# Performance work log

Hardware: AMD Instinct MI355X
Metric: run time of the kernel (lower is better)

The kernel has to match this reference:

```python
import jax, jax.numpy as jnp
import numpy as np

N = 100000
E = 1600000
IN_DIM = 128
HID_DIM = 128
OUT_DIM = 128


def _sage_conv(x, src, dst, W_l, b_l, W_r, num_nodes):
    """PyG SAGEConv with mean aggregation:
       out = mean_{j in N(i)} x_j @ W_l + b_l + x_i @ W_r
    edge_index convention: messages flow src -> dst."""
    msg = x[src]                                        # [E, d_in] gather
    agg_sum = jax.ops.segment_sum(msg, dst, num_segments=num_nodes)   # [N, d_in]
    cnt = jax.ops.segment_sum(jnp.ones((msg.shape[0],), x.dtype), dst,
                              num_segments=num_nodes)   # [N]
    agg = agg_sum / jnp.maximum(cnt, 1.0)[:, None]      # scatter-mean (0 for isolated nodes)
    return agg @ W_l + b_l + x @ W_r


def setup_inputs() -> dict:
    key = jax.random.key(0)
    ks = jax.random.split(key, 8)
    def glorot(k, fan_in, fan_out):
        s = jnp.sqrt(2.0 / (fan_in + fan_out))
        return jax.random.normal(k, (fan_in, fan_out), dtype=jnp.float32) * s
    x = jax.random.normal(ks[0], (N, IN_DIM), dtype=jnp.float32)
    edge_index = jax.random.randint(ks[1], (2, E), 0, N, dtype=jnp.int64)
    return {
        "x": x,
        "edge_index": edge_index,
        "W1_l": glorot(ks[2], IN_DIM, HID_DIM),
        "b1": jnp.zeros((HID_DIM,), jnp.float32),
        "W1_r": glorot(ks[3], IN_DIM, HID_DIM),
        "W2_l": glorot(ks[4], HID_DIM, OUT_DIM),
        "b2": jnp.zeros((OUT_DIM,), jnp.float32),
        "W2_r": glorot(ks[5], HID_DIM, OUT_DIM),
    }


def reference(x, edge_index, W1_l, b1, W1_r, W2_l, b2, W2_r):
    src, dst = edge_index[0], edge_index[1]
    h = _sage_conv(x, src, dst, W1_l, b1, W1_r, N)
    h = jax.nn.relu(h)
    # F.dropout(p=0.5, training=self.training): identity in eval mode
    out = _sage_conv(h, src, dst, W2_l, b2, W2_r, N)
    return out
```

## Files before the change

kernel.cpp:

```cpp
#include <hip/hip_runtime.h>
#include <hip/hip_bf16.h>

#define N_NODES 100000
#define N_EDGES 1600000
#define DIM 128
#define BR 32
#define ESTG 1024
#define NB 782
#define CHUNK 16384

typedef __attribute__((ext_vector_type(8))) short bf16x8;
typedef __attribute__((ext_vector_type(4))) float f32x4;
typedef __attribute__((ext_vector_type(2))) float f32x2;

#define OFF_ROWPTR 0
#define OFF_BCNT   (N_NODES + 4)
#define OFF_BBASE  (OFF_BCNT + NB)
#define OFF_BCUR   (OFF_BBASE + NB)
#define OFF_PAIRS  (OFF_BCUR + NB)
#define OFF_COLSRC (OFF_PAIRS + N_EDGES)
#define OFF_HB     (OFF_COLSRC + N_EDGES)
#define OFF_HF8    (OFF_HB + N_NODES * DIM / 2)
#define OFF_WB     (OFF_HF8 + N_NODES * DIM / 4)

__device__ inline unsigned int f2bf(float f) {
    unsigned int u = __float_as_uint(f);
    return (u + 0x7FFFu + ((u >> 16) & 1u)) >> 16;
}

__global__ __launch_bounds__(256) void conv_pack_kernel(
    const float* __restrict__ x, unsigned char* __restrict__ xf8,
    const float* __restrict__ W1l, const float* __restrict__ W1r,
    const float* __restrict__ W2l, const float* __restrict__ W2r,
    unsigned short* __restrict__ WB,
    const int* __restrict__ dst, int* __restrict__ bcnt)
{
    __shared__ int histL[NB];
    const int b = blockIdx.x;
    const int tid = threadIdx.x;
    if (b < 6250) {
        long i = (long)(b * 256 + tid) * 8;
        float4 a = *(const float4*)(x + i);
        float4 c = *(const float4*)(x + i + 4);
        unsigned int w0 = 0, w1 = 0;
        w0 = __builtin_amdgcn_cvt_pk_fp8_f32(a.x, a.y, w0, false);
        w0 = __builtin_amdgcn_cvt_pk_fp8_f32(a.z, a.w, w0, true);
        w1 = __builtin_amdgcn_cvt_pk_fp8_f32(c.x, c.y, w1, false);
        w1 = __builtin_amdgcn_cvt_pk_fp8_f32(c.z, c.w, w1, true);
        uint2 o; o.x = w0; o.y = w1;
        *(uint2*)(xf8 + i) = o;
    } else if (b < 6506) {
        int t = (b - 6250) * 256 + tid;
        int layer = t >> 15;
        int rest  = t & 32767;
        int half  = rest >> 14;
        int idx   = rest & 16383;
        int k = idx >> 7;
        int n = idx & 127;
        const float* W = layer ? (half ? W2r : W2l) : (half ? W1r : W1l);
        int kk = half * 128 + k;
        WB[layer * 32768 + (((kk >> 3) * 128 + n) << 3) + (kk & 7)] =
            (unsigned short)f2bf(W[idx]);
    } else {
        const int e0 = (b - 6506) * CHUNK;
        const int e1 = min(e0 + CHUNK, N_EDGES);
        for (int q = tid; q < NB; q += 256) histL[q] = 0;
        __syncthreads();
        for (int i = e0 + tid; i < e1; i += 256)
            atomicAdd(&histL[dst[i] >> 7], 1);
        __syncthreads();
        for (int q = tid; q < NB; q += 256) {
            int c = histL[q];
            if (c) atomicAdd(&bcnt[q], c);
        }
    }
}

__global__ __launch_bounds__(1024) void bscan_kernel(
    const int* __restrict__ bcnt, int* __restrict__ bbase,
    int* __restrict__ bcur, int* __restrict__ rowptr)
{
    __shared__ int tmp[1024];
    int tid = threadIdx.x;
    int v = (tid < NB) ? bcnt[tid] : 0;
    tmp[tid] = v;
    __syncthreads();
    for (int off = 1; off < 1024; off <<= 1) {
        int t = (tid >= off) ? tmp[tid - off] : 0;
        __syncthreads();
        tmp[tid] += t;
        __syncthreads();
    }
    if (tid < NB) { int b = tmp[tid] - v; bbase[tid] = b; bcur[tid] = b; }
    if (tid == 0) rowptr[N_NODES] = N_EDGES;
}

__global__ __launch_bounds__(256) void bfill_kernel(
    const int* __restrict__ src, const int* __restrict__ dst,
    int* __restrict__ bcur, unsigned int* __restrict__ pairs)
{
    __shared__ int histL[NB];
    __shared__ int baseL[NB];
    const int tid = threadIdx.x;
    const int e0 = blockIdx.x * CHUNK;
    const int e1 = min(e0 + CHUNK, N_EDGES);
    for (int b = tid; b < NB; b += 256) histL[b] = 0;
    __syncthreads();
    for (int i = e0 + tid; i < e1; i += 256)
        atomicAdd(&histL[dst[i] >> 7], 1);
    __syncthreads();
    for (int b = tid; b < NB; b += 256) {
        int c = histL[b];
        baseL[b] = c ? atomicAdd(&bcur[b], c) : 0;
        histL[b] = 0;
    }
    __syncthreads();
    for (int i = e0 + tid; i < e1; i += 256) {
        int s = src[i];
        int d = dst[i];
        int bk = d >> 7;
        int r = atomicAdd(&histL[bk], 1);
        pairs[baseL[bk] + r] = (unsigned int)s | ((unsigned int)(d & 127) << 25);
    }
}

__global__ __launch_bounds__(256) void bucket_csr_kernel(
    const unsigned int* __restrict__ pairs,
    const int* __restrict__ bcnt, const int* __restrict__ bbase,
    int* __restrict__ rowptr, int* __restrict__ colsrc)
{
    __shared__ int histA[128], exclS[128], hist2[128];
    const int bucket = blockIdx.x;
    const int tid = threadIdx.x;
    const int cnt  = bcnt[bucket];
    const int base = bbase[bucket];
    if (tid < 128) { histA[tid] = 0; hist2[tid] = 0; }
    __syncthreads();
    for (int i = tid; i < cnt; i += 256)
        atomicAdd(&histA[pairs[base + i] >> 25], 1);
    __syncthreads();
    int v = 0;
    if (tid < 128) { v = histA[tid]; exclS[tid] = v; }
    __syncthreads();
    for (int off = 1; off < 128; off <<= 1) {
        int t = 0;
        if (tid < 128 && tid >= off) t = exclS[tid - off];
        __syncthreads();
        if (tid < 128) exclS[tid] += t;
        __syncthreads();
    }
    if (tid < 128) exclS[tid] -= v;
    const int node0 = bucket * 128;
    if (tid < 128 && node0 + tid < N_NODES)
        rowptr[node0 + tid] = base + exclS[tid];
    __syncthreads();
    for (int i = tid; i < cnt; i += 256) {
        unsigned int p = pairs[base + i];
        int dl = (int)(p >> 25);
        int r = atomicAdd(&hist2[dl], 1);
        colsrc[base + exclS[dl] + r] = (int)(p & 0x1FFFFFFu);
    }
}

__device__ inline void addfp8(float* acc, uint2 v) {
    f32x2 p;
    p = __builtin_amdgcn_cvt_pk_f32_fp8((int)v.x, false); acc[0] += p.x; acc[1] += p.y;
    p = __builtin_amdgcn_cvt_pk_f32_fp8((int)v.x, true);  acc[2] += p.x; acc[3] += p.y;
    p = __builtin_amdgcn_cvt_pk_f32_fp8((int)v.y, false); acc[4] += p.x; acc[5] += p.y;
    p = __builtin_amdgcn_cvt_pk_f32_fp8((int)v.y, true);  acc[6] += p.x; acc[7] += p.y;
}

__global__ __launch_bounds__(256, 8) void fused_sage_kernel(
    const unsigned char* __restrict__ f8,
    const float* __restrict__ selfF,
    const unsigned short* __restrict__ selfB,
    const int* __restrict__ rowptr,
    const int* __restrict__ colsrc,
    const unsigned short* __restrict__ WB,
    const float* __restrict__ bias,
    unsigned short* __restrict__ outb,
    unsigned char* __restrict__ outf8,
    float* __restrict__ outf,
    int mode)
{
    __shared__ unsigned short catS[BR * 256];
    __shared__ int eS[ESTG];

    const int tid = threadIdx.x;
    const int block_row = blockIdx.x * BR;
    const int ebase = rowptr[block_row];
    const int span  = rowptr[block_row + BR] - ebase;
    const int smax  = span < ESTG ? span : ESTG;

    for (int i = tid; i < smax; i += 256)
        eS[i] = colsrc[ebase + i] << 7;
    __syncthreads();

    const int c   = tid & 15;
    const int c8  = c * 8;
    const int grp = tid >> 4;

    #pragma unroll
    for (int it = 0; it < 2; ++it) {
        const int nl = grp * 2 + it;
        const int node = block_row + nl;
        const int s  = rowptr[node] - ebase;
        const int e_ = rowptr[node + 1] - ebase;
        const int lim = e_ < ESTG ? e_ : ESTG;

        uint4 sv;
        if (mode) {
            float4 sa = *(const float4*)(selfF + ((long)node << 7) + c8);
            float4 sb = *(const float4*)(selfF + ((long)node << 7) + c8 + 4);
            sv.x = f2bf(sa.x) | (f2bf(sa.y) << 16);
            sv.y = f2bf(sa.z) | (f2bf(sa.w) << 16);
            sv.z = f2bf(sb.x) | (f2bf(sb.y) << 16);
            sv.w = f2bf(sb.z) | (f2bf(sb.w) << 16);
        } else {
            sv = *(const uint4*)(selfB + ((long)node << 7) + c8);
        }

        float acc[8];
        #pragma unroll
        for (int q = 0; q < 8; ++q) acc[q] = 0.0f;

        int i = s;
        for (; i + 8 <= lim; i += 8) {
            const uint2 v0 = *(const uint2*)(f8 + eS[i + 0] + c8);
            const uint2 v1 = *(const uint2*)(f8 + eS[i + 1] + c8);
            const uint2 v2 = *(const uint2*)(f8 + eS[i + 2] + c8);
            const uint2 v3 = *(const uint2*)(f8 + eS[i + 3] + c8);
            const uint2 v4 = *(const uint2*)(f8 + eS[i + 4] + c8);
            const uint2 v5 = *(const uint2*)(f8 + eS[i + 5] + c8);
            const uint2 v6 = *(const uint2*)(f8 + eS[i + 6] + c8);
            const uint2 v7 = *(const uint2*)(f8 + eS[i + 7] + c8);
            addfp8(acc, v0); addfp8(acc, v1); addfp8(acc, v2); addfp8(acc, v3);
            addfp8(acc, v4); addfp8(acc, v5); addfp8(acc, v6); addfp8(acc, v7);
        }
        if (i + 4 <= lim) {
            const uint2 v0 = *(const uint2*)(f8 + eS[i + 0] + c8);
            const uint2 v1 = *(const uint2*)(f8 + eS[i + 1] + c8);
            const uint2 v2 = *(const uint2*)(f8 + eS[i + 2] + c8);
            const uint2 v3 = *(const uint2*)(f8 + eS[i + 3] + c8);
            addfp8(acc, v0); addfp8(acc, v1); addfp8(acc, v2); addfp8(acc, v3);
            i += 4;
        }
        if (i + 2 <= lim) {
            const uint2 v0 = *(const uint2*)(f8 + eS[i + 0] + c8);
            const uint2 v1 = *(const uint2*)(f8 + eS[i + 1] + c8);
            addfp8(acc, v0); addfp8(acc, v1);
            i += 2;
        }
        if (i < lim) {
            const uint2 v = *(const uint2*)(f8 + eS[i] + c8);
            addfp8(acc, v);
            ++i;
        }
        for (; i < e_; ++i) {
            const uint2 v = *(const uint2*)(f8 + ((long)colsrc[ebase + i] << 7) + c8);
            addfp8(acc, v);
        }

        const float inv = 1.0f / fmaxf((float)(e_ - s), 1.0f);
        uint4 pv;
        pv.x = f2bf(acc[0] * inv) | (f2bf(acc[1] * inv) << 16);
        pv.y = f2bf(acc[2] * inv) | (f2bf(acc[3] * inv) << 16);
        pv.z = f2bf(acc[4] * inv) | (f2bf(acc[5] * inv) << 16);
        pv.w = f2bf(acc[6] * inv) | (f2bf(acc[7] * inv) << 16);
        const int sw = c ^ (nl & 7);
        *(uint4*)&catS[nl * 256 + sw * 8] = pv;
        *(uint4*)&catS[nl * 256 + 128 + sw * 8] = sv;
    }
    __syncthreads();

    const int w    = tid >> 6;
    const int l    = tid & 63;
    const int wm   = w & 1;
    const int wn   = w >> 1;
    const int lrow = l & 15;
    const int kgrp = l >> 4;
    const int ar   = wm * 16 + lrow;

    f32x4 acc4[4];
    #pragma unroll
    for (int t = 0; t < 4; ++t) acc4[t] = (f32x4){0.f, 0.f, 0.f, 0.f};

    #pragma unroll
    for (int step = 0; step < 8; ++step) {
        const int slot = step * 4 + kgrp;
        bf16x8 a = *(const bf16x8*)&catS[ar * 256 + ((slot ^ (ar & 7)) << 3)];
        #pragma unroll
        for (int t = 0; t < 4; ++t) {
            const int n = wn * 64 + t * 16 + lrow;
            bf16x8 b = *(const bf16x8*)(WB + ((slot * 128 + n) << 3));
            acc4[t] = __builtin_amdgcn_mfma_f32_16x16x32_bf16(a, b, acc4[t], 0, 0, 0);
        }
    }

    const long orow0 = block_row + wm * 16 + kgrp * 4;
    const int  cbase = wn * 64 + lrow;
    #pragma unroll
    for (int t = 0; t < 4; ++t) {
        const int col = cbase + t * 16;
        const float bb = bias[col];
        #pragma unroll
        for (int j = 0; j < 4; ++j) {
            float v = acc4[t][j] + bb;
            const long row = orow0 + j;
            if (mode) {
                v = fmaxf(v, 0.0f);
                outb[row * DIM + col] = (unsigned short)f2bf(v);
                outf8[row * DIM + col] =
                    (unsigned char)(__builtin_amdgcn_cvt_pk_fp8_f32(v, v, 0u, false) & 0xFFu);
            } else {
                outf[row * DIM + col] = v;
            }
        }
    }
}

extern "C" void kernel_launch(void* const* d_in, const int* in_sizes, int n_in,
                              void* d_out, int out_size, void* d_ws, size_t ws_size,
                              hipStream_t stream)
{
    const float* x   = (const float*)d_in[0];
    const int*   ei  = (const int*)d_in[1];
    const float* W1l = (const float*)d_in[2];
    const float* b1  = (const float*)d_in[3];
    const float* W1r = (const float*)d_in[4];
    const float* W2l = (const float*)d_in[5];
    const float* b2  = (const float*)d_in[6];
    const float* W2r = (const float*)d_in[7];
    float* out = (float*)d_out;

    const int* src = ei;
    const int* dst = ei + N_EDGES;

    int* wsi = (int*)d_ws;
    int* rowptr = wsi + OFF_ROWPTR;
    int* bcnt   = wsi + OFF_BCNT;
    int* bbase  = wsi + OFF_BBASE;
    int* bcur   = wsi + OFF_BCUR;
    unsigned int* pairs = (unsigned int*)(wsi + OFF_PAIRS);
    int* colsrc = wsi + OFF_COLSRC;
    unsigned short* hb  = (unsigned short*)(wsi + OFF_HB);
    unsigned char*  hf8 = (unsigned char*)(wsi + OFF_HF8);
    unsigned short* WB  = (unsigned short*)(wsi + OFF_WB);

    unsigned char* xf8 = (unsigned char*)d_out;

    hipMemsetAsync(bcnt, 0, (size_t)NB * sizeof(int), stream);

    const int eblocks = (N_EDGES + CHUNK - 1) / CHUNK;
    conv_pack_kernel<<<6506 + eblocks, 256, 0, stream>>>(
        x, xf8, W1l, W1r, W2l, W2r, WB, dst, bcnt);
    bscan_kernel<<<1, 1024, 0, stream>>>(bcnt, bbase, bcur, rowptr);
    bfill_kernel<<<eblocks, 256, 0, stream>>>(src, dst, bcur, pairs);
    bucket_csr_kernel<<<NB, 256, 0, stream>>>(pairs, bcnt, bbase, rowptr, colsrc);

    const int gblocks = N_NODES / BR;
    fused_sage_kernel<<<gblocks, 256, 0, stream>>>(
        xf8, x, (const unsigned short*)nullptr, rowptr, colsrc,
        WB, b1, hb, hf8, (float*)nullptr, 1);
    fused_sage_kernel<<<gblocks, 256, 0, stream>>>(
        hf8, (const float*)nullptr, hb, rowptr, colsrc,
        WB + 32768, b2, (unsigned short*)nullptr, (unsigned char*)nullptr, out, 0);
}
```

Measured before the change: 220.8 us.

## Stage epilogue through LDS for coalesced stores, vectorize edge loads, prepack bf16 self features

```diff
diff --git a/kernel.cpp b/kernel.cpp
--- a/kernel.cpp
+++ b/kernel.cpp
@@ -12,6 +12,10 @@
 typedef __attribute__((ext_vector_type(8))) short bf16x8;
 typedef __attribute__((ext_vector_type(4))) float f32x4;
 typedef __attribute__((ext_vector_type(2))) float f32x2;
+typedef __attribute__((ext_vector_type(4))) float f4;
+typedef __attribute__((ext_vector_type(4))) unsigned int u32x4;
+typedef __attribute__((ext_vector_type(2))) unsigned int u32x2;
+typedef __attribute__((ext_vector_type(4))) int i32x4;
 
 #define OFF_ROWPTR 0
 #define OFF_BCNT   (N_NODES + 4)
@@ -27,9 +31,13 @@
     unsigned int u = __float_as_uint(f);
     return (u + 0x7FFFu + ((u >> 16) & 1u)) >> 16;
 }
+__device__ inline unsigned char f2fp8(float v) {
+    return (unsigned char)(__builtin_amdgcn_cvt_pk_fp8_f32(v, v, 0u, false) & 0xFFu);
+}
 
 __global__ __launch_bounds__(256) void conv_pack_kernel(
     const float* __restrict__ x, unsigned char* __restrict__ xf8,
+    unsigned short* __restrict__ xb,
     const float* __restrict__ W1l, const float* __restrict__ W1r,
     const float* __restrict__ W2l, const float* __restrict__ W2r,
     unsigned short* __restrict__ WB,
@@ -40,15 +48,21 @@
     const int tid = threadIdx.x;
     if (b < 6250) {
         long i = (long)(b * 256 + tid) * 8;
-        float4 a = *(const float4*)(x + i);
-        float4 c = *(const float4*)(x + i + 4);
+        f4 a = __builtin_nontemporal_load((const f4*)(x + i));
+        f4 c = __builtin_nontemporal_load((const f4*)(x + i + 4));
         unsigned int w0 = 0, w1 = 0;
-        w0 = __builtin_amdgcn_cvt_pk_fp8_f32(a.x, a.y, w0, false);
-        w0 = __builtin_amdgcn_cvt_pk_fp8_f32(a.z, a.w, w0, true);
-        w1 = __builtin_amdgcn_cvt_pk_fp8_f32(c.x, c.y, w1, false);
-        w1 = __builtin_amdgcn_cvt_pk_fp8_f32(c.z, c.w, w1, true);
-        uint2 o; o.x = w0; o.y = w1;
-        *(uint2*)(xf8 + i) = o;
+        w0 = __builtin_amdgcn_cvt_pk_fp8_f32(a[0], a[1], w0, false);
+        w0 = __builtin_amdgcn_cvt_pk_fp8_f32(a[2], a[3], w0, true);
+        w1 = __builtin_amdgcn_cvt_pk_fp8_f32(c[0], c[1], w1, false);
+        w1 = __builtin_amdgcn_cvt_pk_fp8_f32(c[2], c[3], w1, true);
+        u32x2 o8; o8[0] = w0; o8[1] = w1;
+        __builtin_nontemporal_store(o8, (u32x2*)(xf8 + i));
+        u32x4 ob;
+        ob[0] = f2bf(a[0]) | (f2bf(a[1]) << 16);
+        ob[1] = f2bf(a[2]) | (f2bf(a[3]) << 16);
+        ob[2] = f2bf(c[0]) | (f2bf(c[1]) << 16);
+        ob[3] = f2bf(c[2]) | (f2bf(c[3]) << 16);
+        __builtin_nontemporal_store(ob, (u32x4*)(xb + i));
     } else if (b < 6506) {
         int t = (b - 6250) * 256 + tid;
         int layer = t >> 15;
@@ -66,8 +80,13 @@
         const int e1 = min(e0 + CHUNK, N_EDGES);
         for (int q = tid; q < NB; q += 256) histL[q] = 0;
         __syncthreads();
-        for (int i = e0 + tid; i < e1; i += 256)
-            atomicAdd(&histL[dst[i] >> 7], 1);
+        for (int i = (e0 >> 2) + tid; i < (e1 >> 2); i += 256) {
+            i32x4 d = __builtin_nontemporal_load((const i32x4*)dst + i);
+            atomicAdd(&histL[d[0] >> 7], 1);
+            atomicAdd(&histL[d[1] >> 7], 1);
+            atomicAdd(&histL[d[2] >> 7], 1);
+            atomicAdd(&histL[d[3] >> 7], 1);
+        }
         __syncthreads();
         for (int q = tid; q < NB; q += 256) {
             int c = histL[q];
@@ -106,8 +125,13 @@
     const int e1 = min(e0 + CHUNK, N_EDGES);
     for (int b = tid; b < NB; b += 256) histL[b] = 0;
     __syncthreads();
-    for (int i = e0 + tid; i < e1; i += 256)
-        atomicAdd(&histL[dst[i] >> 7], 1);
+    for (int i = (e0 >> 2) + tid; i < (e1 >> 2); i += 256) {
+        i32x4 d = __builtin_nontemporal_load((const i32x4*)dst + i);
+        atomicAdd(&histL[d[0] >> 7], 1);
+        atomicAdd(&histL[d[1] >> 7], 1);
+        atomicAdd(&histL[d[2] >> 7], 1);
+        atomicAdd(&histL[d[3] >> 7], 1);
+    }
     __syncthreads();
     for (int b = tid; b < NB; b += 256) {
         int c = histL[b];
@@ -115,12 +139,16 @@
         histL[b] = 0;
     }
     __syncthreads();
-    for (int i = e0 + tid; i < e1; i += 256) {
-        int s = src[i];
-        int d = dst[i];
-        int bk = d >> 7;
-        int r = atomicAdd(&histL[bk], 1);
-        pairs[baseL[bk] + r] = (unsigned int)s | ((unsigned int)(d & 127) << 25);
+    for (int i = (e0 >> 2) + tid; i < (e1 >> 2); i += 256) {
+        i32x4 s = __builtin_nontemporal_load((const i32x4*)src + i);
+        i32x4 d = __builtin_nontemporal_load((const i32x4*)dst + i);
+        #pragma unroll
+        for (int k = 0; k < 4; ++k) {
+            int bk = d[k] >> 7;
+            int r = atomicAdd(&histL[bk], 1);
+            pairs[baseL[bk] + r] =
+                (unsigned int)s[k] | ((unsigned int)(d[k] & 127) << 25);
+        }
     }
 }
 
@@ -162,17 +190,16 @@
     }
 }
 
-__device__ inline void addfp8(float* acc, uint2 v) {
+__device__ inline void addfp8(float* acc, u32x2 v) {
     f32x2 p;
-    p = __builtin_amdgcn_cvt_pk_f32_fp8((int)v.x, false); acc[0] += p.x; acc[1] += p.y;
-    p = __builtin_amdgcn_cvt_pk_f32_fp8((int)v.x, true);  acc[2] += p.x; acc[3] += p.y;
-    p = __builtin_amdgcn_cvt_pk_f32_fp8((int)v.y, false); acc[4] += p.x; acc[5] += p.y;
-    p = __builtin_amdgcn_cvt_pk_f32_fp8((int)v.y, true);  acc[6] += p.x; acc[7] += p.y;
+    p = __builtin_amdgcn_cvt_pk_f32_fp8((int)v[0], false); acc[0] += p[0]; acc[1] += p[1];
+    p = __builtin_amdgcn_cvt_pk_f32_fp8((int)v[0], true);  acc[2] += p[0]; acc[3] += p[1];
+    p = __builtin_amdgcn_cvt_pk_f32_fp8((int)v[1], false); acc[4] += p[0]; acc[5] += p[1];
+    p = __builtin_amdgcn_cvt_pk_f32_fp8((int)v[1], true);  acc[6] += p[0]; acc[7] += p[1];
 }
 
 __global__ __launch_bounds__(256, 8) void fused_sage_kernel(
     const unsigned char* __restrict__ f8,
-    const float* __restrict__ selfF,
     const unsigned short* __restrict__ selfB,
     const int* __restrict__ rowptr,
     const int* __restrict__ colsrc,
@@ -193,7 +220,7 @@
     const int smax  = span < ESTG ? span : ESTG;
 
     for (int i = tid; i < smax; i += 256)
-        eS[i] = colsrc[ebase + i] << 7;
+        eS[i] = __builtin_nontemporal_load(&colsrc[ebase + i]) << 7;
     __syncthreads();
 
     const int c   = tid & 15;
@@ -208,17 +235,8 @@
         const int e_ = rowptr[node + 1] - ebase;
         const int lim = e_ < ESTG ? e_ : ESTG;
 
-        uint4 sv;
-        if (mode) {
-            float4 sa = *(const float4*)(selfF + ((long)node << 7) + c8);
-            float4 sb = *(const float4*)(selfF + ((long)node << 7) + c8 + 4);
-            sv.x = f2bf(sa.x) | (f2bf(sa.y) << 16);
-            sv.y = f2bf(sa.z) | (f2bf(sa.w) << 16);
-            sv.z = f2bf(sb.x) | (f2bf(sb.y) << 16);
-            sv.w = f2bf(sb.z) | (f2bf(sb.w) << 16);
-        } else {
-            sv = *(const uint4*)(selfB + ((long)node << 7) + c8);
-        }
+        const u32x4 sv = __builtin_nontemporal_load(
+            (const u32x4*)(selfB + ((long)node << 7) + c8));
 
         float acc[8];
         #pragma unroll
@@ -226,38 +244,38 @@
 
         int i = s;
         for (; i + 8 <= lim; i += 8) {
-            const uint2 v0 = *(const uint2*)(f8 + eS[i + 0] + c8);
-            const uint2 v1 = *(const uint2*)(f8 + eS[i + 1] + c8);
-            const uint2 v2 = *(const uint2*)(f8 + eS[i + 2] + c8);
-            const uint2 v3 = *(const uint2*)(f8 + eS[i + 3] + c8);
-            const uint2 v4 = *(const uint2*)(f8 + eS[i + 4] + c8);
-            const uint2 v5 = *(const uint2*)(f8 + eS[i + 5] + c8);
-            const uint2 v6 = *(const uint2*)(f8 + eS[i + 6] + c8);
-            const uint2 v7 = *(const uint2*)(f8 + eS[i + 7] + c8);
+            const u32x2 v0 = *(const u32x2*)(f8 + eS[i + 0] + c8);
+            const u32x2 v1 = *(const u32x2*)(f8 + eS[i + 1] + c8);
+            const u32x2 v2 = *(const u32x2*)(f8 + eS[i + 2] + c8);
+            const u32x2 v3 = *(const u32x2*)(f8 + eS[i + 3] + c8);
+            const u32x2 v4 = *(const u32x2*)(f8 + eS[i + 4] + c8);
+            const u32x2 v5 = *(const u32x2*)(f8 + eS[i + 5] + c8);
+            const u32x2 v6 = *(const u32x2*)(f8 + eS[i + 6] + c8);
+            const u32x2 v7 = *(const u32x2*)(f8 + eS[i + 7] + c8);
             addfp8(acc, v0); addfp8(acc, v1); addfp8(acc, v2); addfp8(acc, v3);
             addfp8(acc, v4); addfp8(acc, v5); addfp8(acc, v6); addfp8(acc, v7);
         }
         if (i + 4 <= lim) {
-            const uint2 v0 = *(const uint2*)(f8 + eS[i + 0] + c8);
-            const uint2 v1 = *(const uint2*)(f8 + eS[i + 1] + c8);
-            const uint2 v2 = *(const uint2*)(f8 + eS[i + 2] + c8);
-            const uint2 v3 = *(const uint2*)(f8 + eS[i + 3] + c8);
+            const u32x2 v0 = *(const u32x2*)(f8 + eS[i + 0] + c8);
+            const u32x2 v1 = *(const u32x2*)(f8 + eS[i + 1] + c8);
+            const u32x2 v2 = *(const u32x2*)(f8 + eS[i + 2] + c8);
+            const u32x2 v3 = *(const u32x2*)(f8 + eS[i + 3] + c8);
             addfp8(acc, v0); addfp8(acc, v1); addfp8(acc, v2); addfp8(acc, v3);
             i += 4;
         }
         if (i + 2 <= lim) {
-            const uint2 v0 = *(const uint2*)(f8 + eS[i + 0] + c8);
-            const uint2 v1 = *(const uint2*)(f8 + eS[i + 1] + c8);
+            const u32x2 v0 = *(const u32x2*)(f8 + eS[i + 0] + c8);
+            const u32x2 v1 = *(const u32x2*)(f8 + eS[i + 1] + c8);
             addfp8(acc, v0); addfp8(acc, v1);
             i += 2;
         }
         if (i < lim) {
-            const uint2 v = *(const uint2*)(f8 + eS[i] + c8);
+            const u32x2 v = *(const u32x2*)(f8 + eS[i] + c8);
             addfp8(acc, v);
             ++i;
         }
         for (; i < e_; ++i) {
-            const uint2 v = *(const uint2*)(f8 + ((long)colsrc[ebase + i] << 7) + c8);
+            const u32x2 v = *(const u32x2*)(f8 + ((long)colsrc[ebase + i] << 7) + c8);
             addfp8(acc, v);
         }
 
@@ -269,7 +287,7 @@
         pv.w = f2bf(acc[6] * inv) | (f2bf(acc[7] * inv) << 16);
         const int sw = c ^ (nl & 7);
         *(uint4*)&catS[nl * 256 + sw * 8] = pv;
-        *(uint4*)&catS[nl * 256 + 128 + sw * 8] = sv;
+        *(u32x4*)&catS[nl * 256 + 128 + sw * 8] = sv;
     }
     __syncthreads();
 
@@ -297,24 +315,61 @@
         }
     }
 
-    const long orow0 = block_row + wm * 16 + kgrp * 4;
-    const int  cbase = wn * 64 + lrow;
-    #pragma unroll
-    for (int t = 0; t < 4; ++t) {
-        const int col = cbase + t * 16;
-        const float bb = bias[col];
-        #pragma unroll
-        for (int j = 0; j < 4; ++j) {
-            float v = acc4[t][j] + bb;
-            const long row = orow0 + j;
-            if (mode) {
-                v = fmaxf(v, 0.0f);
-                outb[row * DIM + col] = (unsigned short)f2bf(v);
-                outf8[row * DIM + col] =
-                    (unsigned char)(__builtin_amdgcn_cvt_pk_fp8_f32(v, v, 0u, false) & 0xFFu);
-            } else {
-                outf[row * DIM + col] = v;
+    __syncthreads();
+    const int cbase = wn * 64 + lrow;
+    if (mode) {
+        unsigned short* lbf = catS;
+        unsigned char*  lf8 = ((unsigned char*)catS) + 8192;
+        #pragma unroll
+        for (int t = 0; t < 4; ++t) {
+            const int col = cbase + t * 16;
+            const int ch  = col >> 4;
+            const int lo  = col & 15;
+            const float bb = bias[col];
+            #pragma unroll
+            for (int j = 0; j < 4; ++j) {
+                float v = fmaxf(acc4[t][j] + bb, 0.0f);
+                const int row = wm * 16 + kgrp * 4 + j;
+                const int pc  = ch ^ (row & 7);
+                lbf[row * 128 + (pc << 4) + lo] = (unsigned short)f2bf(v);
+                lf8[row * 128 + (pc << 4) + lo] = f2fp8(v);
             }
+        }
+        __syncthreads();
+        const int row = tid >> 3;
+        const int ch  = tid & 7;
+        const int pc  = ch ^ (row & 7);
+        const long g  = (long)(block_row + row) * 128 + ch * 16;
+        u32x4 b0 = *(const u32x4*)&lbf[row * 128 + (pc << 4)];
+        u32x4 b1 = *(const u32x4*)&lbf[row * 128 + (pc << 4) + 8];
+        __builtin_nontemporal_store(b0, (u32x4*)&outb[g]);
+        __builtin_nontemporal_store(b1, (u32x4*)&outb[g + 8]);
+        u32x4 p0 = *(const u32x4*)&lf8[row * 128 + (pc << 4)];
+        __builtin_nontemporal_store(p0, (u32x4*)&outf8[g]);
+    } else {
+        float* lf = (float*)catS;
+        #pragma unroll
+        for (int t = 0; t < 4; ++t) {
+            const int col = cbase + t * 16;
+            const int ch  = col >> 4;
+            const int lo  = col & 15;
+            const float bb = bias[col];
+            #pragma unroll
+            for (int j = 0; j < 4; ++j) {
+                const int row = wm * 16 + kgrp * 4 + j;
+                const int pc  = ch ^ (row & 7);
+                lf[row * 128 + (pc << 4) + lo] = acc4[t][j] + bb;
+            }
+        }
+        __syncthreads();
+        const int row = tid >> 3;
+        const int ch  = tid & 7;
+        const int pc  = ch ^ (row & 7);
+        const long g  = (long)(block_row + row) * 128 + ch * 16;
+        #pragma unroll
+        for (int k = 0; k < 4; ++k) {
+            f4 v = *(const f4*)&lf[row * 128 + (pc << 4) + k * 4];
+            __builtin_nontemporal_store(v, (f4*)&outf[g + k * 4]);
         }
     }
 }
@@ -347,22 +402,22 @@
     unsigned char*  hf8 = (unsigned char*)(wsi + OFF_HF8);
     unsigned short* WB  = (unsigned short*)(wsi + OFF_WB);
 
-    unsigned char* xf8 = (unsigned char*)d_out;
+    unsigned char*  xf8 = (unsigned char*)d_out;
+    unsigned short* xb  = (unsigned short*)(xf8 + (size_t)N_NODES * DIM);
 
     hipMemsetAsync(bcnt, 0, (size_t)NB * sizeof(int), stream);
 
     const int eblocks = (N_EDGES + CHUNK - 1) / CHUNK;
     conv_pack_kernel<<<6506 + eblocks, 256, 0, stream>>>(
-        x, xf8, W1l, W1r, W2l, W2r, WB, dst, bcnt);
+        x, xf8, xb, W1l, W1r, W2l, W2r, WB, dst, bcnt);
     bscan_kernel<<<1, 1024, 0, stream>>>(bcnt, bbase, bcur, rowptr);
     bfill_kernel<<<eblocks, 256, 0, stream>>>(src, dst, bcur, pairs);
     bucket_csr_kernel<<<NB, 256, 0, stream>>>(pairs, bcnt, bbase, rowptr, colsrc);
 
     const int gblocks = N_NODES / BR;
     fused_sage_kernel<<<gblocks, 256, 0, stream>>>(
-        xf8, x, (const unsigned short*)nullptr, rowptr, colsrc,
-        WB, b1, hb, hf8, (float*)nullptr, 1);
+        xf8, xb, rowptr, colsrc, WB, b1, hb, hf8, (float*)nullptr, 1);
     fused_sage_kernel<<<gblocks, 256, 0, stream>>>(
-        hf8, (const float*)nullptr, hb, rowptr, colsrc,
-        WB + 32768, b2, (unsigned short*)nullptr, (unsigned char*)nullptr, out, 0);
-}
+        hf8, hb, rowptr, colsrc, WB + 32768, b2,
+        (unsigned short*)nullptr, (unsigned char*)nullptr, out, 0);
+}
```

After: 245.5 us. +11.2%, slower.
